# Kernel optimization log

Measured on AMD Instinct MI355X. Metric: run time of the kernel, lower is better.

## Reference

```python
import jax, jax.numpy as jnp
import numpy as np

B = 8
SHAPE = (4, 16, 16)   # latent video shape; S = prod = 1024
S = 1024
AE = 64               # ae_embed_dim
D = 768               # embed_dim
F = 3072              # mlp_dim
H = 12                # num_heads (heads are re-merged before the score matmul!)
L = 12                # num_layers
C = 17                # n_classes
OUT = 1024            # out_dim
EPS = 1e-6
HD = D // H


def setup_inputs() -> dict:
    key = jax.random.key(0)
    ks = iter(jax.random.split(key, 64))

    def p(shape, s=0.02):
        return jax.random.normal(next(ks), shape, jnp.float32) * s

    inp = {
        'x': jax.random.normal(next(ks), (B, *SHAPE, AE), jnp.float32),
        'mask': jnp.tril(jnp.ones((S, S), bool)),  # causal
        'label': jax.nn.one_hot(jax.random.randint(next(ks), (B,), 0, C), C, dtype=jnp.float32),
        'dense_in_w': p((D, AE)), 'dense_in_b': jnp.zeros((D,), jnp.float32),
        'sos': p((D,)),
        # BroadcastPositionBiases: embed_dim=768 split into 3 chunks of 256
        'pos0': p((SHAPE[0], D // 3)), 'pos1': p((SHAPE[1], D // 3)), 'pos2': p((SHAPE[2], D // 3)),
        'ln1_sw': p((L, D, C)), 'ln1_bw': p((L, D, C)),
        'qkv_w': p((L, 3 * D, D)), 'qkv_b': jnp.zeros((L, 3 * D), jnp.float32),
        'ao1_w': p((L, D, D)), 'ao1_b': jnp.zeros((L, D), jnp.float32),  # DotProductAttention.out_proj
        'ao2_w': p((L, D, D)), 'ao2_b': jnp.zeros((L, D), jnp.float32),  # MultiHeadAttention.out_proj
        'ln2_sw': p((L, D, C)), 'ln2_bw': p((L, D, C)),
        'mlp_w1': p((L, F, D)), 'mlp_b1': jnp.zeros((L, F), jnp.float32),
        'mlp_w2': p((L, D, F)), 'mlp_b2': jnp.zeros((L, D), jnp.float32),
        'lnf_sw': p((D, C)), 'lnf_bw': p((D, C)),
        'out_w': p((OUT, D)), 'out_b': jnp.zeros((OUT,), jnp.float32),
    }
    return inp


def cond_ln(x, cond, sw, bw):
    # conditional LayerNorm: mul = rsqrt(var+eps)*(1+Linear(cond)), bias = Linear(cond)
    mean = jnp.mean(x, axis=-1, keepdims=True)
    var = jnp.mean((x - mean) ** 2, axis=-1, keepdims=True)
    scale = cond @ sw.T   # [B, D]
    bias = cond @ bw.T    # [B, D]
    mul = jax.lax.rsqrt(var + EPS) * (1.0 + scale[:, None, :])
    return (x - mean) * mul + bias[:, None, :]


def pos_bias(embs, shape):
    n = len(shape)
    outs = []
    for i, e in enumerate(embs):
        sh = [1] * n + [e.shape[-1]]
        sh[i] = shape[i]
        outs.append(jnp.broadcast_to(e.reshape(sh), tuple(shape) + (e.shape[-1],)))
    return jnp.concatenate(outs, axis=-1).reshape(-1, sum(e.shape[-1] for e in embs))  # [S, D]


def attn_block(h, mask, qkv_w, qkv_b, o1_w, o1_b, o2_w, o2_b):
    Bn, Sn, Dn = h.shape
    qkv = h @ qkv_w.T + qkv_b                       # [B, S, 3D]
    qkv = qkv.reshape(Bn, Sn, H, 3 * HD)            # per-head [q|k|v] layout
    q = qkv[..., :HD].reshape(Bn, Sn, Dn)           # heads re-merged BEFORE scores
    k = qkv[..., HD:2 * HD].reshape(Bn, Sn, Dn)
    v = qkv[..., 2 * HD:].reshape(Bn, Sn, Dn)
    # NOTE: scaling uses full embed_dim (module quirk), not head_dim
    scores = jnp.einsum('bqd,bkd->bqk', q * (float(Dn) ** -0.5), k)
    scores = jnp.where(mask[None, :, :], scores, -jnp.inf)
    w = jax.nn.softmax(scores, axis=-1)
    out = jnp.einsum('bqk,bkd->bqd', w, v)
    out = out @ o1_w.T + o1_b                        # DotProductAttention.out_proj
    out = out @ o2_w.T + o2_b                        # MultiHeadAttention.out_proj (applied twice)
    return out


def _forward(x, mask, label, dense_in_w, dense_in_b, sos, pos0, pos1, pos2,
             ln1_sw, ln1_bw, qkv_w, qkv_b, ao1_w, ao1_b, ao2_w, ao2_b,
             ln2_sw, ln2_bw, mlp_w1, mlp_b1, mlp_w2, mlp_b2,
             lnf_sw, lnf_bw, out_w, out_b):
    Bn = x.shape[0]
    old_shape = x.shape[1:-1]
    h = x.reshape(Bn, -1, x.shape[-1]) @ dense_in_w.T + dense_in_b   # [B, S, D]
    # right shift with learned SOS token
    h = jnp.concatenate([jnp.broadcast_to(sos, (Bn, 1, D)), h[:, :-1]], axis=1)
    pb = pos_bias([pos0, pos1, pos2], old_shape)                     # [S, D]
    h = h + pb[None, :h.shape[1]]
    for l in range(L):
        hn = cond_ln(h, label, ln1_sw[l], ln1_bw[l])
        h = h + attn_block(hn, mask, qkv_w[l], qkv_b[l], ao1_w[l], ao1_b[l], ao2_w[l], ao2_b[l])
        hn = cond_ln(h, label, ln2_sw[l], ln2_bw[l])
        m = hn @ mlp_w1[l].T + mlp_b1[l]
        m = jax.nn.sigmoid(1.702 * m) * m           # GELU2
        m = m @ mlp_w2[l].T + mlp_b2[l]
        h = h + m
    h = cond_ln(h, label, lnf_sw, lnf_bw)
    out = h @ out_w.T + out_b                        # [B, S, OUT]
    return out.reshape(Bn, *old_shape, out.shape[-1])


def reference(x, mask, label, dense_in_w, dense_in_b, sos, pos0, pos1, pos2,
              ln1_sw, ln1_bw, qkv_w, qkv_b, ao1_w, ao1_b, ao2_w, ao2_b,
              ln2_sw, ln2_bw, mlp_w1, mlp_b1, mlp_w2, mlp_b2,
              lnf_sw, lnf_bw, out_w, out_b):
    return _forward(x, mask, label, dense_in_w, dense_in_b, sos, pos0, pos1, pos2,
                    ln1_sw, ln1_bw, qkv_w, qkv_b, ao1_w, ao1_b, ao2_w, ao2_b,
                    ln2_sw, ln2_bw, mlp_w1, mlp_b1, mlp_w2, mlp_b2,
                    lnf_sw, lnf_bw, out_w, out_b)
```

## Files before the change

kernel.cpp:

```cpp
#include <hip/hip_runtime.h>

typedef __bf16 bf16;
typedef __bf16 bf16x8 __attribute__((ext_vector_type(8)));
typedef __bf16 bf16x4 __attribute__((ext_vector_type(4)));
typedef float  f32x4  __attribute__((ext_vector_type(4)));

#define DEV __device__ __forceinline__

DEV void gload_lds16(const bf16* g, bf16* l) {
    __builtin_amdgcn_global_load_lds(
        (__attribute__((address_space(1))) void*)g,
        (__attribute__((address_space(3))) void*)l, 16, 0, 0);
}

enum { M_QKV, M_SCORES, M_PV, M_BIAS, M_RESID, M_GELU, M_OUT };

template<int MODE>
__global__ __launch_bounds__(256)
void gemm_k(const bf16* __restrict__ A, const bf16* __restrict__ B,
            int M, int N, int K,
            long long batchA, long long batchB, long long batchC,
            const float* __restrict__ bias,
            bf16* __restrict__ Cb, float* __restrict__ Cf,
            bf16* __restrict__ qp, bf16* __restrict__ kp, bf16* __restrict__ vp)
{
    const int bm = blockIdx.x, bn = blockIdx.y, bz = blockIdx.z;
    int kTiles = K >> 5;

    const int tid = threadIdx.x, wid = tid >> 6, lane = tid & 63;
    const bf16* Ab = A + (long long)bz * batchA + (long long)bm * 128 * K;
    const bf16* Bb = B + (long long)bz * batchB + (long long)bn * 128 * K;

    __shared__ __align__(16) bf16 sA[2][4096];
    __shared__ __align__(16) bf16 sB[2][4096];

    const int srow = wid * 16 + (lane >> 2);
    const int scol = (lane & 3) * 8;
    const long long aoff = (long long)srow * K + scol;

    auto stage = [&](int buf, int kt) {
        const bf16* ga = Ab + (long long)kt * 32;
        const bf16* gb = Bb + (long long)kt * 32;
        gload_lds16(ga + aoff,            &sA[buf][(wid * 16) * 32]);
        gload_lds16(ga + aoff + 64LL * K, &sA[buf][(64 + wid * 16) * 32]);
        gload_lds16(gb + aoff,            &sB[buf][(wid * 16) * 32]);
        gload_lds16(gb + aoff + 64LL * K, &sB[buf][(64 + wid * 16) * 32]);
    };

    f32x4 acc[4][4];
#pragma unroll
    for (int m = 0; m < 4; ++m)
#pragma unroll
        for (int n = 0; n < 4; ++n) acc[m][n] = (f32x4){0.f, 0.f, 0.f, 0.f};

    stage(0, 0);
    __syncthreads();

    const int wr = wid >> 1, wc = wid & 1;
    const int arow = wr * 64 + (lane & 15);
    const int brow = wc * 64 + (lane & 15);
    const int koff = (lane >> 4) * 8;

    for (int kt = 0; kt < kTiles; ++kt) {
        const int cur = kt & 1;
        if (kt + 1 < kTiles) stage(cur ^ 1, kt + 1);
        bf16x8 af[4], bfr[4];
#pragma unroll
        for (int m = 0; m < 4; ++m)
            af[m] = *(const bf16x8*)&sA[cur][(arow + m * 16) * 32 + koff];
#pragma unroll
        for (int n = 0; n < 4; ++n)
            bfr[n] = *(const bf16x8*)&sB[cur][(brow + n * 16) * 32 + koff];
#pragma unroll
        for (int m = 0; m < 4; ++m)
#pragma unroll
            for (int n = 0; n < 4; ++n)
                acc[m][n] = __builtin_amdgcn_mfma_f32_16x16x32_bf16(af[m], bfr[n], acc[m][n], 0, 0, 0);
        __syncthreads();
    }

    const int cr0 = bm * 128 + wr * 64 + (lane >> 4) * 4;
    const int cc0 = bn * 128 + wc * 64 + (lane & 15);
#pragma unroll
    for (int m = 0; m < 4; ++m) {
#pragma unroll
        for (int n = 0; n < 4; ++n) {
            const int col = cc0 + n * 16;
#pragma unroll
            for (int r = 0; r < 4; ++r) {
                const int row = cr0 + m * 16 + r;
                float v = acc[m][n][r];
                if (MODE == M_QKV) {
                    v += bias[col];
                    int hd = col / 192, rr = col % 192;
                    int b = row >> 10, s = row & 1023;
                    if (rr < 64)
                        qp[(long long)row * 768 + hd * 64 + rr] = (bf16)(v * 0.03608439182435161f);
                    else if (rr < 128)
                        kp[(long long)row * 768 + hd * 64 + (rr - 64)] = (bf16)v;
                    else
                        vp[((long long)b * 768 + hd * 64 + (rr - 128)) * 1024 + s] = (bf16)v;
                } else if (MODE == M_GELU) {
                    float xg = v + bias[col];
                    Cb[(long long)row * N + col] = (bf16)(xg / (1.f + __expf(-1.702f * xg)));
                } else {
                    Cf[(long long)row * N + col] = v + bias[col];
                }
            }
        }
    }
}

template<int MODE>
__global__ __launch_bounds__(256)
void gemm64_k(const bf16* __restrict__ A, const bf16* __restrict__ B,
              int M, int N, int K,
              long long batchA, long long batchB, long long batchC,
              const float* __restrict__ bias,
              bf16* __restrict__ Cb, float* __restrict__ Cf)
{
    const int bm = blockIdx.x, bn = blockIdx.y, bz = blockIdx.z;
    if (MODE == M_SCORES && 2 * bn > bm) return;
    int kTiles = K >> 5;
    if (MODE == M_PV) {
        int lim = 2 * bm + 2;
        if (lim < kTiles) kTiles = lim;
    }

    const int tid = threadIdx.x, wid = tid >> 6, lane = tid & 63;
    const bf16* Ab = A + (long long)bz * batchA + (long long)bm * 64 * K;
    const bf16* Bb = B + (long long)bz * batchB + (long long)bn * 128 * K;

    __shared__ __align__(16) bf16 sA[2][2048];
    __shared__ __align__(16) bf16 sB[2][4096];

    const int srow = wid * 16 + (lane >> 2);
    const int scol = (lane & 3) * 8;
    const long long aoff = (long long)srow * K + scol;

    auto stage = [&](int buf, int kt) {
        const bf16* ga = Ab + (long long)kt * 32;
        const bf16* gb = Bb + (long long)kt * 32;
        gload_lds16(ga + aoff,            &sA[buf][(wid * 16) * 32]);
        gload_lds16(gb + aoff,            &sB[buf][(wid * 16) * 32]);
        gload_lds16(gb + aoff + 64LL * K, &sB[buf][(64 + wid * 16) * 32]);
    };

    f32x4 acc[2][4];
#pragma unroll
    for (int m = 0; m < 2; ++m)
#pragma unroll
        for (int n = 0; n < 4; ++n) acc[m][n] = (f32x4){0.f, 0.f, 0.f, 0.f};

    stage(0, 0);
    __syncthreads();

    const int wr = wid >> 1, wc = wid & 1;
    const int arow = wr * 32 + (lane & 15);
    const int brow = wc * 64 + (lane & 15);
    const int koff = (lane >> 4) * 8;

    for (int kt = 0; kt < kTiles; ++kt) {
        const int cur = kt & 1;
        if (kt + 1 < kTiles) stage(cur ^ 1, kt + 1);
        bf16x8 af[2], bfr[4];
#pragma unroll
        for (int m = 0; m < 2; ++m)
            af[m] = *(const bf16x8*)&sA[cur][(arow + m * 16) * 32 + koff];
#pragma unroll
        for (int n = 0; n < 4; ++n)
            bfr[n] = *(const bf16x8*)&sB[cur][(brow + n * 16) * 32 + koff];
#pragma unroll
        for (int m = 0; m < 2; ++m)
#pragma unroll
            for (int n = 0; n < 4; ++n)
                acc[m][n] = __builtin_amdgcn_mfma_f32_16x16x32_bf16(af[m], bfr[n], acc[m][n], 0, 0, 0);
        __syncthreads();
    }

    const int cr0 = bm * 64 + wr * 32 + (lane >> 4) * 4;
    const int cc0 = bn * 128 + wc * 64 + (lane & 15);
#pragma unroll
    for (int m = 0; m < 2; ++m) {
#pragma unroll
        for (int n = 0; n < 4; ++n) {
            const int col = cc0 + n * 16;
#pragma unroll
            for (int r = 0; r < 4; ++r) {
                const int row = cr0 + m * 16 + r;
                float v = acc[m][n][r];
                if (MODE == M_SCORES || MODE == M_PV) {
                    Cb[(long long)bz * batchC + (long long)row * N + col] = (bf16)v;
                } else if (MODE == M_BIAS) {
                    Cb[(long long)row * N + col] = (bf16)(v + bias[col]);
                } else if (MODE == M_RESID) {
                    long long idx = (long long)row * N + col;
                    Cf[idx] += v + bias[col];
                } else {
                    Cf[(long long)row * N + col] = v + bias[col];
                }
            }
        }
    }
}

__global__ __launch_bounds__(256)
void cvt_bf16_k(const float* __restrict__ in, bf16* __restrict__ out, int n4)
{
    int i = blockIdx.x * 256 + threadIdx.x;
    if (i >= n4) return;
    float4 f = ((const float4*)in)[i];
    bf16x4 o = { (bf16)f.x, (bf16)f.y, (bf16)f.z, (bf16)f.w };
    ((bf16x4*)out)[i] = o;
}

__global__ __launch_bounds__(256)
void cond_proj_k(const float* __restrict__ label, const float* __restrict__ sw,
                 const float* __restrict__ bw, float* __restrict__ scale,
                 float* __restrict__ bias, int total)
{
    int idx = blockIdx.x * 256 + threadIdx.x;
    if (idx >= total) return;
    int l = idx / 6144;
    int rem = idx - l * 6144;
    int b = rem / 768, d = rem - (rem / 768) * 768;
    const float* lab = label + b * 17;
    const float* swp = sw + ((long long)l * 768 + d) * 17;
    const float* bwp = bw + ((long long)l * 768 + d) * 17;
    float s = 0.f, bb = 0.f;
#pragma unroll
    for (int c = 0; c < 17; ++c) { float lv = lab[c]; s += lv * swp[c]; bb += lv * bwp[c]; }
    scale[idx] = s;
    bias[idx]  = bb;
}

__global__ __launch_bounds__(256)
void shift_pos_k(const float* __restrict__ xe, const float* __restrict__ sos,
                 const float* __restrict__ p0, const float* __restrict__ p1,
                 const float* __restrict__ p2, float* __restrict__ h)
{
    const int s = blockIdx.x, b = blockIdx.y;
    const int i0 = s >> 8, i1 = (s >> 4) & 15, i2 = s & 15;
    const float* xr = xe + ((long long)b * 1024 + (s - 1)) * 768;
#pragma unroll
    for (int j = 0; j < 3; ++j) {
        const int d = j * 256 + threadIdx.x;
        float v = (s == 0) ? sos[d] : xr[d];
        float pbv = (d < 256) ? p0[i0 * 256 + d]
                  : (d < 512) ? p1[i1 * 256 + (d - 256)]
                              : p2[i2 * 256 + (d - 512)];
        h[((long long)b * 1024 + s) * 768 + d] = v + pbv;
    }
}

__global__ __launch_bounds__(256)
void cond_ln_k(const float* __restrict__ h, const float* __restrict__ scale,
               const float* __restrict__ bias, bf16* __restrict__ out)
{
    const long long row = (long long)blockIdx.y * 1024 + blockIdx.x;
    const int b = blockIdx.y;
    const float* hr = h + row * 768;
    float v[3], sum = 0.f, sq = 0.f;
#pragma unroll
    for (int j = 0; j < 3; ++j) {
        v[j] = hr[j * 256 + threadIdx.x];
        sum += v[j]; sq += v[j] * v[j];
    }
    __shared__ float sm[8];
#pragma unroll
    for (int o = 32; o; o >>= 1) { sum += __shfl_down(sum, o); sq += __shfl_down(sq, o); }
    const int wid = threadIdx.x >> 6;
    if ((threadIdx.x & 63) == 0) { sm[wid] = sum; sm[4 + wid] = sq; }
    __syncthreads();
    sum = sm[0] + sm[1] + sm[2] + sm[3];
    sq  = sm[4] + sm[5] + sm[6] + sm[7];
    const float mean = sum * (1.f / 768.f);
    const float var  = sq * (1.f / 768.f) - mean * mean;
    const float rs   = rsqrtf(var + 1e-6f);
    const float* sc = scale + (long long)b * 768;
    const float* bi = bias  + (long long)b * 768;
    bf16* orow = out + row * 768;
#pragma unroll
    for (int j = 0; j < 3; ++j) {
        const int d = j * 256 + threadIdx.x;
        orow[d] = (bf16)((v[j] - mean) * rs * (1.f + sc[d]) + bi[d]);
    }
}

__global__ __launch_bounds__(256)
void softmax_k(bf16* __restrict__ P)
{
    const int i = blockIdx.x, b = blockIdx.y;
    bf16* row = P + ((long long)b * 1024 + i) * 1024;
    const int len = i + 1;
    float v[4], mx = -1e30f;
#pragma unroll
    for (int j = 0; j < 4; ++j) {
        int c = j * 256 + threadIdx.x;
        v[j] = (c < len) ? (float)row[c] : -1e30f;
        mx = fmaxf(mx, v[j]);
    }
    __shared__ float sm[8];
#pragma unroll
    for (int o = 32; o; o >>= 1) mx = fmaxf(mx, __shfl_down(mx, o));
    const int wid = threadIdx.x >> 6;
    if ((threadIdx.x & 63) == 0) sm[wid] = mx;
    __syncthreads();
    mx = fmaxf(fmaxf(sm[0], sm[1]), fmaxf(sm[2], sm[3]));
    float s = 0.f;
#pragma unroll
    for (int j = 0; j < 4; ++j) {
        v[j] = __expf(v[j] - mx);
        s += ((j * 256 + threadIdx.x) < len) ? v[j] : 0.f;
    }
#pragma unroll
    for (int o = 32; o; o >>= 1) s += __shfl_down(s, o);
    if ((threadIdx.x & 63) == 0) sm[4 + wid] = s;
    __syncthreads();
    s = sm[4] + sm[5] + sm[6] + sm[7];
    const float inv = 1.f / s;
#pragma unroll
    for (int j = 0; j < 4; ++j) {
        int c = j * 256 + threadIdx.x;
        row[c] = (c < len) ? (bf16)(v[j] * inv) : (bf16)0.f;
    }
}

__global__ __launch_bounds__(256)
void fill_k(float* o, int n, float v)
{
    int i = blockIdx.x * 256 + threadIdx.x;
    if (i < n) o[i] = v;
}

extern "C" void kernel_launch(void* const* d_in, const int* in_sizes, int n_in,
                              void* d_out, int out_size, void* d_ws, size_t ws_size,
                              hipStream_t stream)
{
    (void)in_sizes; (void)n_in;
    const float* x     = (const float*)d_in[0];
    const float* label = (const float*)d_in[2];
    const float* dw    = (const float*)d_in[3];
    const float* db    = (const float*)d_in[4];
    const float* sos   = (const float*)d_in[5];
    const float* p0    = (const float*)d_in[6];
    const float* p1    = (const float*)d_in[7];
    const float* p2    = (const float*)d_in[8];
    const float* ln1sw = (const float*)d_in[9];
    const float* ln1bw = (const float*)d_in[10];
    const float* qkvw  = (const float*)d_in[11];
    const float* qkvb  = (const float*)d_in[12];
    const float* ao1w  = (const float*)d_in[13];
    const float* ao1b  = (const float*)d_in[14];
    const float* ao2w  = (const float*)d_in[15];
    const float* ao2b  = (const float*)d_in[16];
    const float* ln2sw = (const float*)d_in[17];
    const float* ln2bw = (const float*)d_in[18];
    const float* m1w   = (const float*)d_in[19];
    const float* m1b   = (const float*)d_in[20];
    const float* m2w   = (const float*)d_in[21];
    const float* m2b   = (const float*)d_in[22];
    const float* lnfsw = (const float*)d_in[23];
    const float* lnfbw = (const float*)d_in[24];
    const float* outw  = (const float*)d_in[25];
    const float* outb  = (const float*)d_in[26];
    float* out = (float*)d_out;

    char* p = (char*)d_ws;
    char* pend = (char*)d_ws + ws_size;
    auto alloc = [&](size_t bytes) { void* r = (void*)p; p += (bytes + 255) & ~(size_t)255; return r; };
    float* h    = (float*)alloc(8192LL * 768 * 4);
    bf16*  hn   = (bf16*) alloc(8192LL * 768 * 2);
    bf16*  q    = (bf16*) alloc(8192LL * 768 * 2);
    bf16*  kbuf = (bf16*) alloc(8192LL * 768 * 2);
    bf16*  vT   = (bf16*) alloc(8192LL * 768 * 2);
    bf16*  P    = (bf16*) alloc(8LL * 1024 * 1024 * 2);
    bf16*  attn = (bf16*) alloc(8192LL * 768 * 2);
    bf16*  o1o  = (bf16*) alloc(8192LL * 768 * 2);
    bf16*  mb   = (bf16*) alloc(8192LL * 3072 * 2);
    bf16*  wout = (bf16*) alloc(1024LL * 768 * 2);
    float* s1   = (float*)alloc(12LL * 8 * 768 * 4);
    float* b1   = (float*)alloc(12LL * 8 * 768 * 4);
    float* s2   = (float*)alloc(12LL * 8 * 768 * 4);
    float* b2   = (float*)alloc(12LL * 8 * 768 * 4);
    float* sf   = (float*)alloc(8LL * 768 * 4);
    float* bfb  = (float*)alloc(8LL * 768 * 4);

    size_t base_needed = (size_t)(p - (char*)d_ws);
    if (base_needed + 16LL * 1024 * 1024 > ws_size) {
        fill_k<<<(out_size + 255) / 256, 256, 0, stream>>>(out, out_size, 1e9f);
        return;
    }

    const long long SZ_QKV = 2304LL * 768, SZ_O = 768LL * 768, SZ_M = 3072LL * 768;
    size_t all_bytes = (size_t)(12 * (SZ_QKV + 2 * SZ_O + 2 * SZ_M)) * 2;
    bool allw = ((size_t)(p - (char*)d_ws) + all_bytes + 4096 <= ws_size);

    bf16 *wqkvA, *wo1A, *wo2A, *wm1A, *wm2A;
    if (allw) {
        wqkvA = (bf16*)alloc(12 * SZ_QKV * 2);
        wo1A  = (bf16*)alloc(12 * SZ_O * 2);
        wo2A  = (bf16*)alloc(12 * SZ_O * 2);
        wm1A  = (bf16*)alloc(12 * SZ_M * 2);
        wm2A  = (bf16*)alloc(12 * SZ_M * 2);
    } else {
        wqkvA = (bf16*)alloc(SZ_QKV * 2);
        wo1A  = (bf16*)alloc(SZ_O * 2);
        wo2A  = (bf16*)alloc(SZ_O * 2);
        wm1A  = (bf16*)alloc(SZ_M * 2);
        wm2A  = (bf16*)alloc(SZ_M * 2);
    }

    bf16*  xbf  = (bf16*)P;
    bf16*  dwbf = (bf16*)(P + 1024 * 1024);
    float* xe   = (float*)mb;

    cvt_bf16_k<<<1024 * 768 / 4 / 256, 256, 0, stream>>>(outw, wout, 1024 * 768 / 4);
    cond_proj_k<<<(12 * 8 * 768 + 255) / 256, 256, 0, stream>>>(label, ln1sw, ln1bw, s1, b1, 12 * 8 * 768);
    cond_proj_k<<<(12 * 8 * 768 + 255) / 256, 256, 0, stream>>>(label, ln2sw, ln2bw, s2, b2, 12 * 8 * 768);
    cond_proj_k<<<(8 * 768 + 255) / 256, 256, 0, stream>>>(label, lnfsw, lnfbw, sf, bfb, 8 * 768);

    if (allw) {
        cvt_bf16_k<<<(int)(12 * SZ_QKV / 4 / 256), 256, 0, stream>>>(qkvw, wqkvA, (int)(12 * SZ_QKV / 4));
        cvt_bf16_k<<<(int)(12 * SZ_O / 4 / 256),   256, 0, stream>>>(ao1w, wo1A,  (int)(12 * SZ_O / 4));
        cvt_bf16_k<<<(int)(12 * SZ_O / 4 / 256),   256, 0, stream>>>(ao2w, wo2A,  (int)(12 * SZ_O / 4));
        cvt_bf16_k<<<(int)(12 * SZ_M / 4 / 256),   256, 0, stream>>>(m1w,  wm1A,  (int)(12 * SZ_M / 4));
        cvt_bf16_k<<<(int)(12 * SZ_M / 4 / 256),   256, 0, stream>>>(m2w,  wm2A,  (int)(12 * SZ_M / 4));
    }

    cvt_bf16_k<<<8192 * 64 / 4 / 256, 256, 0, stream>>>(x, xbf, 8192 * 64 / 4);
    cvt_bf16_k<<<768 * 64 / 4 / 256, 256, 0, stream>>>(dw, dwbf, 768 * 64 / 4);
    gemm_k<M_OUT><<<dim3(64, 6, 1), 256, 0, stream>>>(
        xbf, dwbf, 8192, 768, 64, 0, 0, 0, db, nullptr, xe, nullptr, nullptr, nullptr);
    shift_pos_k<<<dim3(1024, 8), 256, 0, stream>>>(xe, sos, p0, p1, p2, h);

    for (int l = 0; l < 12; ++l) {
        bf16 *wqkv, *wo1, *wo2, *wm1, *wm2;
        if (allw) {
            wqkv = wqkvA + (long long)l * SZ_QKV;
            wo1  = wo1A  + (long long)l * SZ_O;
            wo2  = wo2A  + (long long)l * SZ_O;
            wm1  = wm1A  + (long long)l * SZ_M;
            wm2  = wm2A  + (long long)l * SZ_M;
        } else {
            wqkv = wqkvA; wo1 = wo1A; wo2 = wo2A; wm1 = wm1A; wm2 = wm2A;
            cvt_bf16_k<<<(int)(SZ_QKV / 4 / 256), 256, 0, stream>>>(qkvw + (long long)l * SZ_QKV, wqkv, (int)(SZ_QKV / 4));
            cvt_bf16_k<<<(int)(SZ_O / 4 / 256),   256, 0, stream>>>(ao1w + (long long)l * SZ_O,   wo1,  (int)(SZ_O / 4));
            cvt_bf16_k<<<(int)(SZ_O / 4 / 256),   256, 0, stream>>>(ao2w + (long long)l * SZ_O,   wo2,  (int)(SZ_O / 4));
            cvt_bf16_k<<<(int)(SZ_M / 4 / 256),   256, 0, stream>>>(m1w  + (long long)l * SZ_M,   wm1,  (int)(SZ_M / 4));
            cvt_bf16_k<<<(int)(SZ_M / 4 / 256),   256, 0, stream>>>(m2w  + (long long)l * SZ_M,   wm2,  (int)(SZ_M / 4));
        }

        cond_ln_k<<<dim3(1024, 8), 256, 0, stream>>>(h, s1 + (long long)l * 6144, b1 + (long long)l * 6144, hn);

        gemm_k<M_QKV><<<dim3(64, 18, 1), 256, 0, stream>>>(
            hn, wqkv, 8192, 2304, 768, 0, 0, 0,
            qkvb + (long long)l * 2304, nullptr, nullptr, q, kbuf, vT);

        gemm64_k<M_SCORES><<<dim3(16, 8, 8), 256, 0, stream>>>(
            q, kbuf, 1024, 1024, 768, 1024LL * 768, 1024LL * 768, 1024LL * 1024,
            nullptr, P, nullptr);

        softmax_k<<<dim3(1024, 8), 256, 0, stream>>>(P);

        gemm64_k<M_PV><<<dim3(16, 6, 8), 256, 0, stream>>>(
            P, vT, 1024, 768, 1024, 1024LL * 1024, 768LL * 1024, 1024LL * 768,
            nullptr, attn, nullptr);

        gemm64_k<M_BIAS><<<dim3(128, 6, 1), 256, 0, stream>>>(
            attn, wo1, 8192, 768, 768, 0, 0, 0,
            ao1b + (long long)l * 768, o1o, nullptr);

        gemm64_k<M_RESID><<<dim3(128, 6, 1), 256, 0, stream>>>(
            o1o, wo2, 8192, 768, 768, 0, 0, 0,
            ao2b + (long long)l * 768, nullptr, h);

        cond_ln_k<<<dim3(1024, 8), 256, 0, stream>>>(h, s2 + (long long)l * 6144, b2 + (long long)l * 6144, hn);

        gemm_k<M_GELU><<<dim3(64, 24, 1), 256, 0, stream>>>(
            hn, wm1, 8192, 3072, 768, 0, 0, 0,
            m1b + (long long)l * 3072, mb, nullptr, nullptr, nullptr, nullptr);

        gemm64_k<M_RESID><<<dim3(128, 6, 1), 256, 0, stream>>>(
            mb, wm2, 8192, 768, 3072, 0, 0, 0,
            m2b + (long long)l * 768, nullptr, h);
    }

    cond_ln_k<<<dim3(1024, 8), 256, 0, stream>>>(h, sf, bfb, hn);
    gemm64_k<M_OUT><<<dim3(128, 8, 1), 256, 0, stream>>>(
        hn, wout, 8192, 1024, 768, 0, 0, 0,
        outb, nullptr, out);
}
```

Baseline: 4.476 ms.

## Merge the two attention output projections into one weight and split-K the residual GEMMs

```diff
diff --git a/kernel.cpp b/kernel.cpp
--- a/kernel.cpp
+++ b/kernel.cpp
@@ -13,13 +13,13 @@
         (__attribute__((address_space(3))) void*)l, 16, 0, 0);
 }
 
-enum { M_QKV, M_SCORES, M_PV, M_BIAS, M_RESID, M_GELU, M_OUT };
+enum { M_QKV, M_SCORES, M_PV, M_RSPLIT, M_GELU, M_OUT, M_WM };
 
 template<int MODE>
 __global__ __launch_bounds__(256)
 void gemm_k(const bf16* __restrict__ A, const bf16* __restrict__ B,
             int M, int N, int K,
-            long long batchA, long long batchB, long long batchC,
+            long long batchA, long long batchB, long long batchC, int ksplit,
             const float* __restrict__ bias,
             bf16* __restrict__ Cb, float* __restrict__ Cf,
             bf16* __restrict__ qp, bf16* __restrict__ kp, bf16* __restrict__ vp)
@@ -28,8 +28,16 @@
     int kTiles = K >> 5;
 
     const int tid = threadIdx.x, wid = tid >> 6, lane = tid & 63;
-    const bf16* Ab = A + (long long)bz * batchA + (long long)bm * 128 * K;
-    const bf16* Bb = B + (long long)bz * batchB + (long long)bn * 128 * K;
+    const bf16* Ab;
+    const bf16* Bb;
+    if (MODE == M_RSPLIT) {
+        kTiles /= ksplit;
+        Ab = A + (long long)bm * 128 * K + (long long)bz * kTiles * 32;
+        Bb = B + (long long)bn * 128 * K + (long long)bz * kTiles * 32;
+    } else {
+        Ab = A + (long long)bz * batchA + (long long)bm * 128 * K;
+        Bb = B + (long long)bz * batchB + (long long)bn * 128 * K;
+    }
 
     __shared__ __align__(16) bf16 sA[2][4096];
     __shared__ __align__(16) bf16 sB[2][4096];
@@ -103,6 +111,11 @@
                 } else if (MODE == M_GELU) {
                     float xg = v + bias[col];
                     Cb[(long long)row * N + col] = (bf16)(xg / (1.f + __expf(-1.702f * xg)));
+                } else if (MODE == M_RSPLIT) {
+                    float add = v + (bz == 0 ? bias[col] : 0.f);
+                    atomicAdd(&Cf[(long long)row * N + col], add);
+                } else if (MODE == M_WM) {
+                    Cb[(long long)bz * batchC + (long long)row * N + col] = (bf16)v;
                 } else {
                     Cf[(long long)row * N + col] = v + bias[col];
                 }
@@ -191,11 +204,6 @@
                 float v = acc[m][n][r];
                 if (MODE == M_SCORES || MODE == M_PV) {
                     Cb[(long long)bz * batchC + (long long)row * N + col] = (bf16)v;
-                } else if (MODE == M_BIAS) {
-                    Cb[(long long)row * N + col] = (bf16)(v + bias[col]);
-                } else if (MODE == M_RESID) {
-                    long long idx = (long long)row * N + col;
-                    Cf[idx] += v + bias[col];
                 } else {
                     Cf[(long long)row * N + col] = v + bias[col];
                 }
@@ -212,6 +220,45 @@
     float4 f = ((const float4*)in)[i];
     bf16x4 o = { (bf16)f.x, (bf16)f.y, (bf16)f.z, (bf16)f.w };
     ((bf16x4*)out)[i] = o;
+}
+
+__global__ __launch_bounds__(256)
+void transpose_cvt_k(const float* __restrict__ in, bf16* __restrict__ out, int n)
+{
+    __shared__ float t[32][33];
+    const int l = blockIdx.z;
+    const int r0 = blockIdx.y * 32, c0 = blockIdx.x * 32;
+    const float* src = in + (long long)l * n * n;
+    bf16* dst = out + (long long)l * n * n;
+    const int tx = threadIdx.x & 31, ty = threadIdx.x >> 5;
+#pragma unroll
+    for (int i = 0; i < 32; i += 8)
+        t[ty + i][tx] = src[(long long)(r0 + ty + i) * n + c0 + tx];
+    __syncthreads();
+#pragma unroll
+    for (int i = 0; i < 32; i += 8)
+        dst[(long long)(c0 + ty + i) * n + r0 + tx] = (bf16)t[tx][ty + i];
+}
+
+__global__ __launch_bounds__(256)
+void bias_merge_k(const float* __restrict__ o2w, const float* __restrict__ o1b,
+                  const float* __restrict__ o2b, float* __restrict__ bm, int total)
+{
+    const int wid = threadIdx.x >> 6, lane = threadIdx.x & 63;
+    const int idx = blockIdx.x * 4 + wid;
+    if (idx >= total) return;
+    const int l = idx / 768, a = idx - l * 768;
+    const float* wrow = o2w + ((long long)l * 768 + a) * 768;
+    const float* brow = o1b + (long long)l * 768;
+    float s = 0.f;
+#pragma unroll
+    for (int j = 0; j < 12; ++j) {
+        int c = j * 64 + lane;
+        s += wrow[c] * brow[c];
+    }
+#pragma unroll
+    for (int o = 32; o; o >>= 1) s += __shfl_down(s, o);
+    if (lane == 0) bm[idx] = s + o2b[(long long)l * 768 + a];
 }
 
 __global__ __launch_bounds__(256)
@@ -367,7 +414,6 @@
     float* out = (float*)d_out;
 
     char* p = (char*)d_ws;
-    char* pend = (char*)d_ws + ws_size;
     auto alloc = [&](size_t bytes) { void* r = (void*)p; p += (bytes + 255) & ~(size_t)255; return r; };
     float* h    = (float*)alloc(8192LL * 768 * 4);
     bf16*  hn   = (bf16*) alloc(8192LL * 768 * 2);
@@ -376,9 +422,10 @@
     bf16*  vT   = (bf16*) alloc(8192LL * 768 * 2);
     bf16*  P    = (bf16*) alloc(8LL * 1024 * 1024 * 2);
     bf16*  attn = (bf16*) alloc(8192LL * 768 * 2);
-    bf16*  o1o  = (bf16*) alloc(8192LL * 768 * 2);
     bf16*  mb   = (bf16*) alloc(8192LL * 3072 * 2);
     bf16*  wout = (bf16*) alloc(1024LL * 768 * 2);
+    bf16*  wmA  = (bf16*) alloc(12LL * 768 * 768 * 2);
+    float* bmA  = (float*)alloc(12LL * 768 * 4);
     float* s1   = (float*)alloc(12LL * 8 * 768 * 4);
     float* b1   = (float*)alloc(12LL * 8 * 768 * 4);
     float* s2   = (float*)alloc(12LL * 8 * 768 * 4);
@@ -393,27 +440,25 @@
     }
 
     const long long SZ_QKV = 2304LL * 768, SZ_O = 768LL * 768, SZ_M = 3072LL * 768;
-    size_t all_bytes = (size_t)(12 * (SZ_QKV + 2 * SZ_O + 2 * SZ_M)) * 2;
+    size_t all_bytes = (size_t)(12 * (SZ_QKV + 2 * SZ_M)) * 2;
     bool allw = ((size_t)(p - (char*)d_ws) + all_bytes + 4096 <= ws_size);
 
-    bf16 *wqkvA, *wo1A, *wo2A, *wm1A, *wm2A;
+    bf16 *wqkvA, *wm1A, *wm2A;
     if (allw) {
         wqkvA = (bf16*)alloc(12 * SZ_QKV * 2);
-        wo1A  = (bf16*)alloc(12 * SZ_O * 2);
-        wo2A  = (bf16*)alloc(12 * SZ_O * 2);
         wm1A  = (bf16*)alloc(12 * SZ_M * 2);
         wm2A  = (bf16*)alloc(12 * SZ_M * 2);
     } else {
         wqkvA = (bf16*)alloc(SZ_QKV * 2);
-        wo1A  = (bf16*)alloc(SZ_O * 2);
-        wo2A  = (bf16*)alloc(SZ_O * 2);
         wm1A  = (bf16*)alloc(SZ_M * 2);
         wm2A  = (bf16*)alloc(SZ_M * 2);
     }
 
-    bf16*  xbf  = (bf16*)P;
-    bf16*  dwbf = (bf16*)(P + 1024 * 1024);
-    float* xe   = (float*)mb;
+    bf16*  xbf   = (bf16*)P;
+    bf16*  dwbf  = (bf16*)P + 524288;
+    bf16*  wo2bf = (bf16*)P + 1048576;
+    float* xe    = (float*)mb;
+    bf16*  o1t   = mb + 12582912;
 
     cvt_bf16_k<<<1024 * 768 / 4 / 256, 256, 0, stream>>>(outw, wout, 1024 * 768 / 4);
     cond_proj_k<<<(12 * 8 * 768 + 255) / 256, 256, 0, stream>>>(label, ln1sw, ln1bw, s1, b1, 12 * 8 * 768);
@@ -422,31 +467,32 @@
 
     if (allw) {
         cvt_bf16_k<<<(int)(12 * SZ_QKV / 4 / 256), 256, 0, stream>>>(qkvw, wqkvA, (int)(12 * SZ_QKV / 4));
-        cvt_bf16_k<<<(int)(12 * SZ_O / 4 / 256),   256, 0, stream>>>(ao1w, wo1A,  (int)(12 * SZ_O / 4));
-        cvt_bf16_k<<<(int)(12 * SZ_O / 4 / 256),   256, 0, stream>>>(ao2w, wo2A,  (int)(12 * SZ_O / 4));
         cvt_bf16_k<<<(int)(12 * SZ_M / 4 / 256),   256, 0, stream>>>(m1w,  wm1A,  (int)(12 * SZ_M / 4));
         cvt_bf16_k<<<(int)(12 * SZ_M / 4 / 256),   256, 0, stream>>>(m2w,  wm2A,  (int)(12 * SZ_M / 4));
     }
+
+    cvt_bf16_k<<<(int)(12 * SZ_O / 4 / 256), 256, 0, stream>>>(ao2w, wo2bf, (int)(12 * SZ_O / 4));
+    transpose_cvt_k<<<dim3(24, 24, 12), 256, 0, stream>>>(ao1w, o1t, 768);
+    gemm_k<M_WM><<<dim3(6, 6, 12), 256, 0, stream>>>(
+        wo2bf, o1t, 768, 768, 768, SZ_O, SZ_O, SZ_O, 1,
+        nullptr, wmA, nullptr, nullptr, nullptr, nullptr);
+    bias_merge_k<<<(12 * 768 + 3) / 4, 256, 0, stream>>>(ao2w, ao1b, ao2b, bmA, 12 * 768);
 
     cvt_bf16_k<<<8192 * 64 / 4 / 256, 256, 0, stream>>>(x, xbf, 8192 * 64 / 4);
     cvt_bf16_k<<<768 * 64 / 4 / 256, 256, 0, stream>>>(dw, dwbf, 768 * 64 / 4);
     gemm_k<M_OUT><<<dim3(64, 6, 1), 256, 0, stream>>>(
-        xbf, dwbf, 8192, 768, 64, 0, 0, 0, db, nullptr, xe, nullptr, nullptr, nullptr);
+        xbf, dwbf, 8192, 768, 64, 0, 0, 0, 1, db, nullptr, xe, nullptr, nullptr, nullptr);
     shift_pos_k<<<dim3(1024, 8), 256, 0, stream>>>(xe, sos, p0, p1, p2, h);
 
     for (int l = 0; l < 12; ++l) {
-        bf16 *wqkv, *wo1, *wo2, *wm1, *wm2;
+        bf16 *wqkv, *wm1, *wm2;
         if (allw) {
             wqkv = wqkvA + (long long)l * SZ_QKV;
-            wo1  = wo1A  + (long long)l * SZ_O;
-            wo2  = wo2A  + (long long)l * SZ_O;
             wm1  = wm1A  + (long long)l * SZ_M;
             wm2  = wm2A  + (long long)l * SZ_M;
         } else {
-            wqkv = wqkvA; wo1 = wo1A; wo2 = wo2A; wm1 = wm1A; wm2 = wm2A;
+            wqkv = wqkvA; wm1 = wm1A; wm2 = wm2A;
             cvt_bf16_k<<<(int)(SZ_QKV / 4 / 256), 256, 0, stream>>>(qkvw + (long long)l * SZ_QKV, wqkv, (int)(SZ_QKV / 4));
-            cvt_bf16_k<<<(int)(SZ_O / 4 / 256),   256, 0, stream>>>(ao1w + (long long)l * SZ_O,   wo1,  (int)(SZ_O / 4));
-            cvt_bf16_k<<<(int)(SZ_O / 4 / 256),   256, 0, stream>>>(ao2w + (long long)l * SZ_O,   wo2,  (int)(SZ_O / 4));
             cvt_bf16_k<<<(int)(SZ_M / 4 / 256),   256, 0, stream>>>(m1w  + (long long)l * SZ_M,   wm1,  (int)(SZ_M / 4));
             cvt_bf16_k<<<(int)(SZ_M / 4 / 256),   256, 0, stream>>>(m2w  + (long long)l * SZ_M,   wm2,  (int)(SZ_M / 4));
         }
@@ -454,7 +500,7 @@
         cond_ln_k<<<dim3(1024, 8), 256, 0, stream>>>(h, s1 + (long long)l * 6144, b1 + (long long)l * 6144, hn);
 
         gemm_k<M_QKV><<<dim3(64, 18, 1), 256, 0, stream>>>(
-            hn, wqkv, 8192, 2304, 768, 0, 0, 0,
+            hn, wqkv, 8192, 2304, 768, 0, 0, 0, 1,
             qkvb + (long long)l * 2304, nullptr, nullptr, q, kbuf, vT);
 
         gemm64_k<M_SCORES><<<dim3(16, 8, 8), 256, 0, stream>>>(
@@ -467,23 +513,19 @@
             P, vT, 1024, 768, 1024, 1024LL * 1024, 768LL * 1024, 1024LL * 768,
             nullptr, attn, nullptr);
 
-        gemm64_k<M_BIAS><<<dim3(128, 6, 1), 256, 0, stream>>>(
-            attn, wo1, 8192, 768, 768, 0, 0, 0,
-            ao1b + (long long)l * 768, o1o, nullptr);
-
-        gemm64_k<M_RESID><<<dim3(128, 6, 1), 256, 0, stream>>>(
-            o1o, wo2, 8192, 768, 768, 0, 0, 0,
-            ao2b + (long long)l * 768, nullptr, h);
+        gemm_k<M_RSPLIT><<<dim3(64, 6, 2), 256, 0, stream>>>(
+            attn, wmA + (long long)l * SZ_O, 8192, 768, 768, 0, 0, 0, 2,
+            bmA + (long long)l * 768, nullptr, h, nullptr, nullptr, nullptr);
 
         cond_ln_k<<<dim3(1024, 8), 256, 0, stream>>>(h, s2 + (long long)l * 6144, b2 + (long long)l * 6144, hn);
 
         gemm_k<M_GELU><<<dim3(64, 24, 1), 256, 0, stream>>>(
-            hn, wm1, 8192, 3072, 768, 0, 0, 0,
+            hn, wm1, 8192, 3072, 768, 0, 0, 0, 1,
             m1b + (long long)l * 3072, mb, nullptr, nullptr, nullptr, nullptr);
 
-        gemm64_k<M_RESID><<<dim3(128, 6, 1), 256, 0, stream>>>(
-            mb, wm2, 8192, 768, 3072, 0, 0, 0,
-            m2b + (long long)l * 768, nullptr, h);
+        gemm_k<M_RSPLIT><<<dim3(64, 6, 4), 256, 0, stream>>>(
+            mb, wm2, 8192, 768, 3072, 0, 0, 0, 4,
+            m2b + (long long)l * 768, nullptr, h, nullptr, nullptr, nullptr);
     }
 
     cond_ln_k<<<dim3(1024, 8), 256, 0, stream>>>(h, sf, bfb, hn);
```

New measurement: 4.879 ms. +9.0%, slower.
